# Performance work log

Hardware: AMD Instinct MI355X
Metric: run time of the kernel (lower is better)

Reference implementation:

```python
import jax, jax.numpy as jnp
import numpy as np

B, S, DM, H, HD = 2, 4096, 768, 12, 64
SCALING = HD ** -0.5
LN_EPS = 1e-12
ROPE_BASE = 10000.0


def rotate_half(x):
    x1, x2 = jnp.split(x, 2, axis=-1)
    return jnp.concatenate([-x2, x1], axis=-1)


def setup_inputs() -> dict:
    key = jax.random.key(0)
    ks = jax.random.split(key, 8)
    s = 0.02
    hidden_states = jax.random.normal(ks[0], (B, S, DM), dtype=jnp.float32)
    # true rotary tables: inv_freq over head_dim/2, duplicated (HF convention)
    inv_freq = 1.0 / (ROPE_BASE ** (jnp.arange(0, HD, 2, dtype=jnp.float32) / HD))
    freqs = jnp.arange(S, dtype=jnp.float32)[:, None] * inv_freq[None, :]  # [S, HD/2]
    emb = jnp.concatenate([freqs, freqs], axis=-1)                          # [S, HD]
    cos, sin = jnp.cos(emb), jnp.sin(emb)
    return {
        "hidden_states": hidden_states,
        "cos": cos,
        "sin": sin,
        "Wq": jax.random.normal(ks[1], (DM, DM), dtype=jnp.float32) * s,
        "bq": jnp.zeros((DM,), dtype=jnp.float32),
        "Wk": jax.random.normal(ks[2], (DM, DM), dtype=jnp.float32) * s,
        "bk": jnp.zeros((DM,), dtype=jnp.float32),
        "Wv": jax.random.normal(ks[3], (DM, DM), dtype=jnp.float32) * s,
        "bv": jnp.zeros((DM,), dtype=jnp.float32),
        "Wo": jax.random.normal(ks[4], (DM, DM), dtype=jnp.float32) * s,
        "ln_g": jnp.ones((DM,), dtype=jnp.float32),
        "ln_b": jnp.zeros((DM,), dtype=jnp.float32),
    }


def reference(hidden_states, cos, sin, Wq, bq, Wk, bk, Wv, bv, Wo, ln_g, ln_b):
    # QKV projections -> [B, H, S, HD]
    def proj(W, b):
        return (hidden_states @ W.T + b).reshape(B, S, H, HD).transpose(0, 2, 1, 3)
    q, k, v = proj(Wq, bq), proj(Wk, bk), proj(Wv, bv)

    # RoPE (cos/sin broadcast over batch & heads)
    c = cos[None, None, :, :]
    s_ = sin[None, None, :, :]
    q = q * c + rotate_half(q) * s_
    k = k * c + rotate_half(k) * s_

    # Faithful to source: q pre-scaled, then eager attention scales scores again
    q = q * SCALING
    scores = jnp.einsum("bhsd,bhtd->bhst", q, k) * SCALING  # [B,H,S,S]
    probs = jax.nn.softmax(scores.astype(jnp.float32), axis=-1).astype(v.dtype)
    attn = jnp.einsum("bhst,bhtd->bhsd", probs, v)
    attn = attn.transpose(0, 2, 1, 3).reshape(B, S, DM)

    # output dense (no bias) + residual + LayerNorm
    out = attn @ Wo.T + hidden_states
    mu = jnp.mean(out, axis=-1, keepdims=True)
    var = jnp.var(out, axis=-1, keepdims=True)
    out = (out - mu) * jax.lax.rsqrt(var + LN_EPS) * ln_g + ln_b
    return out
```

## Files before the change

kernel.cpp:

```cpp
#include <hip/hip_runtime.h>
#include <math.h>

#define B_   2
#define S_   4096
#define DM_  768
#define H_   12
#define HD_  64
#define M_   (B_ * S_)
#define ROWELEMS ((size_t)M_ * DM_)
#define WELEMS  ((size_t)DM_ * DM_)

#define QSC (1.4426950408889634f / 64.0f)

typedef unsigned short u16;
typedef unsigned int   u32;
typedef __attribute__((ext_vector_type(8))) short  short8;
typedef __attribute__((ext_vector_type(4))) float  floatx4;
typedef __attribute__((ext_vector_type(4))) u32    uint32x4;

__device__ inline u16 f2bf(float f) {
    u32 u = __builtin_bit_cast(u32, f);
    u += 0x7FFF + ((u >> 16) & 1);
    return (u16)(u >> 16);
}
__device__ inline float bf2f(u16 h) {
    return __builtin_bit_cast(float, (u32)h << 16);
}
__device__ inline u32 pk_trunc(float a, float b) {
    return __builtin_amdgcn_perm(__builtin_bit_cast(u32, b),
                                 __builtin_bit_cast(u32, a), 0x07060302);
}

__device__ inline int sw_off(int r, int cg) {
    return (r << 6) + ((cg ^ (r & 7)) << 3);
}

__device__ __forceinline__ void load_lds16(const u16* g, u16* l) {
    __builtin_amdgcn_global_load_lds(
        (const __attribute__((address_space(1))) u32*)g,
        (__attribute__((address_space(3))) u32*)l, 16, 0, 0);
}

__device__ __forceinline__ void drain_vm() {
    __builtin_amdgcn_s_waitcnt(0x0F70);
}
__device__ __forceinline__ void wait_vm4() {
    __builtin_amdgcn_s_waitcnt(0x0F74);
}

__global__ __launch_bounds__(256) void conv_bf16(
    const float* __restrict__ h,  const float* __restrict__ wq,
    const float* __restrict__ wk, const float* __restrict__ wv,
    const float* __restrict__ wo, u16* __restrict__ hb, u16* __restrict__ wb)
{
    const int y = blockIdx.y;
    const float* src; u16* dst; size_t n4;
    if (y == 0)      { src = h;  dst = hb;              n4 = ROWELEMS / 4; }
    else if (y == 1) { src = wq; dst = wb;              n4 = WELEMS / 4; }
    else if (y == 2) { src = wk; dst = wb + WELEMS;     n4 = WELEMS / 4; }
    else if (y == 3) { src = wv; dst = wb + 2 * WELEMS; n4 = WELEMS / 4; }
    else             { src = wo; dst = wb + 3 * WELEMS; n4 = WELEMS / 4; }
    const size_t stride = (size_t)gridDim.x * 256;
    for (size_t i = blockIdx.x * 256 + threadIdx.x; i < n4; i += stride) {
        float4 v = *(const float4*)&src[i * 4];
        u32 p0 = (u32)f2bf(v.x) | ((u32)f2bf(v.y) << 16);
        u32 p1 = (u32)f2bf(v.z) | ((u32)f2bf(v.w) << 16);
        *(uint2*)&dst[i * 4] = make_uint2(p0, p1);
    }
}

__global__ __launch_bounds__(256, 3) void gemm_qkv(
    const u16* __restrict__ A,
    const u16* __restrict__ W0, const u16* __restrict__ W1, const u16* __restrict__ W2,
    const float* __restrict__ b0, const float* __restrict__ b1, const float* __restrict__ b2,
    const float* __restrict__ cosT, const float* __restrict__ sinT,
    u16* __restrict__ Qh, u16* __restrict__ Kh, u16* __restrict__ Vt)
{
    __shared__ __align__(16) u16 As[128 * 64];
    __shared__ __align__(16) u16 Ws[192 * 64];

    const int tid  = threadIdx.x;
    const int wave = tid >> 6, lane = tid & 63;
    const int n16  = lane & 15, quad = lane >> 4;
    const int m0   = blockIdx.y * 128, n0 = blockIdx.x * 192;
    const int z    = blockIdx.z;

    const u16* Wz = (z == 0) ? W0 : (z == 1) ? W1 : W2;
    const float* bz = (z == 0) ? b0 : (z == 1) ? b1 : b2;

    int gao[4], ldsao[4], gwo[6], ldswo[6];
#pragma unroll
    for (int i = 0; i < 4; i++) {
        int g = wave * 256 + i * 64 + lane;
        int r = g >> 3, cg = (g & 7) ^ (r & 7);
        gao[i]   = r * DM_ + cg * 8;
        ldsao[i] = (wave * 256 + i * 64) * 8;
    }
#pragma unroll
    for (int i = 0; i < 6; i++) {
        int g = wave * 384 + i * 64 + lane;
        int r = g >> 3, cg = (g & 7) ^ (r & 7);
        gwo[i]   = r * DM_ + cg * 8;
        ldswo[i] = (wave * 384 + i * 64) * 8;
    }
    const u16* Ap = A  + (size_t)m0 * DM_;
    const u16* Wp = Wz + (size_t)n0 * DM_;

    floatx4 acc[2][12];
#pragma unroll
    for (int i = 0; i < 2; i++)
#pragma unroll
        for (int j = 0; j < 12; j++) acc[i][j] = (floatx4){0.f, 0.f, 0.f, 0.f};

    for (int k0 = 0; k0 < DM_; k0 += 64) {
        __syncthreads();
#pragma unroll
        for (int i = 0; i < 4; i++)
            load_lds16(Ap + k0 + gao[i], &As[ldsao[i]]);
#pragma unroll
        for (int i = 0; i < 6; i++)
            load_lds16(Wp + k0 + gwo[i], &Ws[ldswo[i]]);
        drain_vm();
        __syncthreads();
#pragma unroll
        for (int ks = 0; ks < 2; ks++) {
            short8 af[2];
#pragma unroll
            for (int t = 0; t < 2; t++)
                af[t] = *(const short8*)&As[sw_off(wave * 32 + t * 16 + n16, ks * 4 + quad)];
#pragma unroll
            for (int jh = 0; jh < 2; jh++) {
                short8 bf[6];
#pragma unroll
                for (int j = 0; j < 6; j++)
                    bf[j] = *(const short8*)&Ws[sw_off((jh * 6 + j) * 16 + n16, ks * 4 + quad)];
#pragma unroll
                for (int i = 0; i < 2; i++)
#pragma unroll
                    for (int j = 0; j < 6; j++)
                        acc[i][jh * 6 + j] = __builtin_amdgcn_mfma_f32_16x16x32_bf16(
                            af[i], bf[j], acc[i][jh * 6 + j], 0, 0, 0);
            }
        }
    }

    if (z == 2) {
#pragma unroll
        for (int i = 0; i < 2; i++)
#pragma unroll
            for (int j = 0; j < 12; j++) {
                const int col = n0 + j * 16 + n16;
                const int h = col >> 6, hd = col & 63;
                const int row0 = m0 + wave * 32 + i * 16 + quad * 4;
                const int b = row0 >> 12, s0 = row0 & 4095;
                const float bias = bz[col];
                float v0 = acc[i][j][0] + bias, v1 = acc[i][j][1] + bias;
                float v2 = acc[i][j][2] + bias, v3 = acc[i][j][3] + bias;
                u32 w0 = (u32)f2bf(v0) | ((u32)f2bf(v1) << 16);
                u32 w1 = (u32)f2bf(v2) | ((u32)f2bf(v3) << 16);
                *(uint2*)&Vt[((size_t)(b * H_ + h) * HD_ + hd) * S_ + s0] = make_uint2(w0, w1);
            }
    } else {
        u32* Out32 = (u32*)((z == 0) ? Qh : Kh);
        const float sc_ = (z == 0) ? QSC : 1.0f;
#pragma unroll
        for (int i = 0; i < 2; i++)
#pragma unroll
            for (int jp = 0; jp < 6; jp++) {
                const int j1 = (jp >> 1) * 4 + (jp & 1);
                const int col1 = n0 + j1 * 16 + n16;
                const int h = col1 >> 6, hd1 = col1 & 63;
                const float bias1 = bz[col1], bias2 = bz[col1 + 32];
#pragma unroll
                for (int r = 0; r < 4; r++) {
                    const int row = m0 + wave * 32 + i * 16 + quad * 4 + r;
                    const int b = row >> 12, s = row & 4095;
                    const float c  = cosT[s * HD_ + hd1];
                    const float sn = sinT[s * HD_ + hd1];
                    const float x1 = acc[i][j1][r] + bias1;
                    const float x2 = acc[i][j1 + 2][r] + bias2;
                    const float y1 = (x1 * c - x2 * sn) * sc_;
                    const float y2 = (x2 * c + x1 * sn) * sc_;
                    Out32[(((size_t)(b * H_ + h) * S_ + s) << 5) + hd1] =
                        (u32)f2bf(y1) | ((u32)f2bf(y2) << 16);
                }
            }
    }
}

__global__ __launch_bounds__(256, 3) void flash_mfma(
    const u16* __restrict__ Qh, const u16* __restrict__ Kh,
    const u16* __restrict__ Vt, u16* __restrict__ O)
{
    __shared__ __align__(16) u16 Ks0[64 * 64];
    __shared__ __align__(16) u16 Vs0[64 * 64];
    __shared__ __align__(16) u16 Ks1[64 * 64];
    __shared__ __align__(16) u16 Vs1[64 * 64];
    __shared__ __align__(16) u16 Ks2[64 * 64];
    __shared__ __align__(16) u16 Vs2[64 * 64];

    const int tid  = threadIdx.x;
    const int wave = tid >> 6, lane = tid & 63;
    const int n16  = lane & 15, quad = lane >> 4;
    const int qt   = blockIdx.x;
    const int bh   = blockIdx.y;
    const size_t qk_base = (size_t)bh * S_ * HD_;
    const size_t vt_base = (size_t)bh * HD_ * S_;
    const int q0   = qt * 128;
    const int wrow = wave * 32;

    short8 qf[2][2];
#pragma unroll
    for (int rt = 0; rt < 2; rt++)
#pragma unroll
        for (int ks = 0; ks < 2; ks++)
            qf[rt][ks] = *(const short8*)&Qh[qk_base +
                (size_t)(q0 + wrow + rt * 16 + n16) * HD_ + ks * 32 + quad * 8];

    short8 ones;
#pragma unroll
    for (int j = 0; j < 8; j++) ones[j] = (short)0x3F80;

    int gk_off[2], gv_off[2], ldso[2];
#pragma unroll
    for (int i = 0; i < 2; i++) {
        int g = wave * 128 + i * 64 + lane;
        int r = g >> 3, cg = (g & 7) ^ (r & 7);
        int rk = (r & 0x23) | ((r & 8) << 1) | ((r & 4) << 1) | ((r & 16) >> 2);
        gk_off[i] = rk * HD_ + cg * 8;
        gv_off[i] = r  * S_  + cg * 8;
        ldso[i]   = (wave * 128 + i * 64) * 8;
    }

    floatx4 o_acc[2][4];
    floatx4 o_l[2];
#pragma unroll
    for (int rt = 0; rt < 2; rt++) {
        o_l[rt] = (floatx4){0.f, 0.f, 0.f, 0.f};
#pragma unroll
        for (int dt = 0; dt < 4; dt++) o_acc[rt][dt] = (floatx4){0.f, 0.f, 0.f, 0.f};
    }

    const u16* Kg = Kh + qk_base;
    const u16* Vg = Vt + vt_base;
#define KT (64 * HD_)

#define STAGE(KSRC, VSRC, KDST, VDST)                                   \
    do {                                                                \
        _Pragma("unroll")                                               \
        for (int i_ = 0; i_ < 2; i_++) {                                \
            load_lds16((KSRC) + gk_off[i_], &(KDST)[ldso[i_]]);         \
            load_lds16((VSRC) + gv_off[i_], &(VDST)[ldso[i_]]);         \
        }                                                               \
    } while (0)

#define COMPUTE_TILE(KSB, VSB)                                          \
    do {                                                                \
        floatx4 sct[4][2];                                              \
        _Pragma("unroll")                                               \
        for (int ct = 0; ct < 4; ct++)                                  \
            _Pragma("unroll")                                           \
            for (int rt = 0; rt < 2; rt++)                              \
                sct[ct][rt] = (floatx4){0.f, 0.f, 0.f, 0.f};            \
        _Pragma("unroll")                                               \
        for (int ks = 0; ks < 2; ks++) {                                \
            short8 kf[4];                                               \
            _Pragma("unroll")                                           \
            for (int ct = 0; ct < 4; ct++)                              \
                kf[ct] = *(const short8*)&(KSB)[sw_off(ct * 16 + n16,   \
                                                       ks * 4 + quad)]; \
            _Pragma("unroll")                                           \
            for (int ct = 0; ct < 4; ct++)                              \
                _Pragma("unroll")                                       \
                for (int rt = 0; rt < 2; rt++)                          \
                    sct[ct][rt] = __builtin_amdgcn_mfma_f32_16x16x32_bf16( \
                        kf[ct], qf[rt][ks], sct[ct][rt], 0, 0, 0);      \
        }                                                               \
        short8 pa[2][2];                                                \
        _Pragma("unroll")                                               \
        for (int rt = 0; rt < 2; rt++)                                  \
            _Pragma("unroll")                                           \
            for (int ks = 0; ks < 2; ks++) {                            \
                const floatx4 lo = sct[2 * ks][rt];                     \
                const floatx4 hi = sct[2 * ks + 1][rt];                 \
                uint32x4 w;                                             \
                w[0] = pk_trunc(__builtin_amdgcn_exp2f(lo[0]),          \
                                __builtin_amdgcn_exp2f(lo[1]));         \
                w[1] = pk_trunc(__builtin_amdgcn_exp2f(lo[2]),          \
                                __builtin_amdgcn_exp2f(lo[3]));         \
                w[2] = pk_trunc(__builtin_amdgcn_exp2f(hi[0]),          \
                                __builtin_amdgcn_exp2f(hi[1]));         \
                w[3] = pk_trunc(__builtin_amdgcn_exp2f(hi[2]),          \
                                __builtin_amdgcn_exp2f(hi[3]));         \
                pa[rt][ks] = __builtin_bit_cast(short8, w);             \
            }                                                           \
        _Pragma("unroll")                                               \
        for (int ks = 0; ks < 2; ks++) {                                \
            short8 vb[4];                                               \
            _Pragma("unroll")                                           \
            for (int dt = 0; dt < 4; dt++)                              \
                vb[dt] = *(const short8*)&(VSB)[sw_off(dt * 16 + n16,   \
                                                       ks * 4 + quad)]; \
            _Pragma("unroll")                                           \
            for (int rt = 0; rt < 2; rt++) {                            \
                _Pragma("unroll")                                       \
                for (int dt = 0; dt < 4; dt++)                          \
                    o_acc[rt][dt] = __builtin_amdgcn_mfma_f32_16x16x32_bf16( \
                        pa[rt][ks], vb[dt], o_acc[rt][dt], 0, 0, 0);    \
                o_l[rt] = __builtin_amdgcn_mfma_f32_16x16x32_bf16(      \
                    pa[rt][ks], ones, o_l[rt], 0, 0, 0);                \
            }                                                           \
        }                                                               \
    } while (0)

    STAGE(Kg,      Vg,      Ks0, Vs0);
    STAGE(Kg + KT, Vg + 64, Ks1, Vs1);

    for (int g = 0; g < 21; ++g) {
        wait_vm4();
        __builtin_amdgcn_s_barrier();
        STAGE(Kg + 2 * KT, Vg + 2 * 64, Ks2, Vs2);
        COMPUTE_TILE(Ks0, Vs0);
        Kg += KT; Vg += 64;

        wait_vm4();
        __builtin_amdgcn_s_barrier();
        STAGE(Kg + 2 * KT, Vg + 2 * 64, Ks0, Vs0);
        COMPUTE_TILE(Ks1, Vs1);
        Kg += KT; Vg += 64;

        wait_vm4();
        __builtin_amdgcn_s_barrier();
        if (g < 20)
            STAGE(Kg + 2 * KT, Vg + 2 * 64, Ks1, Vs1);
        COMPUTE_TILE(Ks2, Vs2);
        Kg += KT; Vg += 64;
    }
    drain_vm();
    __builtin_amdgcn_s_barrier();
    COMPUTE_TILE(Ks0, Vs0);
#undef STAGE
#undef COMPUTE_TILE
#undef KT

    const int b = bh / H_, h = bh % H_;
#pragma unroll
    for (int rt = 0; rt < 2; rt++)
#pragma unroll
        for (int r = 0; r < 4; r++) {
            const float inv = 1.0f / o_l[rt][r];
            const int srow = q0 + wrow + rt * 16 + quad * 4 + r;
            u16* Orow = O + ((size_t)b * S_ + srow) * DM_ + h * HD_;
#pragma unroll
            for (int dt = 0; dt < 4; dt++)
                Orow[dt * 16 + n16] = f2bf(o_acc[rt][dt][r] * inv);
        }
}

__global__ __launch_bounds__(256, 4) void gemm_out(
    const u16* __restrict__ A, const u16* __restrict__ W,
    const float* __restrict__ resid, float* __restrict__ Cf)
{
    __shared__ __align__(16) u16 As[64 * 64];
    __shared__ __align__(16) u16 Ws[128 * 64];

    const int tid  = threadIdx.x;
    const int wave = tid >> 6, lane = tid & 63;
    const int n16  = lane & 15, quad = lane >> 4;
    const int wm   = wave >> 1, wn = wave & 1;
    const int m0   = blockIdx.y * 64, n0 = blockIdx.x * 128;

    int gwo[4], ldswo[4], gao[2], ldsao[2];
#pragma unroll
    for (int i = 0; i < 4; i++) {
        int g = wave * 256 + i * 64 + lane;
        int r = g >> 3, cg = (g & 7) ^ (r & 7);
        gwo[i]   = r * DM_ + cg * 8;
        ldswo[i] = (wave * 256 + i * 64) * 8;
    }
#pragma unroll
    for (int i = 0; i < 2; i++) {
        int g = wave * 128 + i * 64 + lane;
        int r = g >> 3, cg = (g & 7) ^ (r & 7);
        gao[i]   = r * DM_ + cg * 8;
        ldsao[i] = (wave * 128 + i * 64) * 8;
    }
    const u16* Wp = W + (size_t)n0 * DM_;
    const u16* Ap = A + (size_t)m0 * DM_;

    floatx4 acc[2][4];
#pragma unroll
    for (int i = 0; i < 2; i++)
#pragma unroll
        for (int j = 0; j < 4; j++) acc[i][j] = (floatx4){0.f, 0.f, 0.f, 0.f};

    for (int k0 = 0; k0 < DM_; k0 += 64) {
        __syncthreads();
#pragma unroll
        for (int i = 0; i < 4; i++)
            load_lds16(Wp + k0 + gwo[i], &Ws[ldswo[i]]);
#pragma unroll
        for (int i = 0; i < 2; i++)
            load_lds16(Ap + k0 + gao[i], &As[ldsao[i]]);
        drain_vm();
        __syncthreads();

#pragma unroll
        for (int ks = 0; ks < 2; ks++) {
            short8 af[2], bf[4];
#pragma unroll
            for (int rt = 0; rt < 2; rt++)
                af[rt] = *(const short8*)&As[sw_off(wm * 32 + rt * 16 + n16, ks * 4 + quad)];
#pragma unroll
            for (int ct = 0; ct < 4; ct++)
                bf[ct] = *(const short8*)&Ws[sw_off(wn * 64 + ct * 16 + n16, ks * 4 + quad)];
#pragma unroll
            for (int rt = 0; rt < 2; rt++)
#pragma unroll
                for (int ct = 0; ct < 4; ct++)
                    acc[rt][ct] = __builtin_amdgcn_mfma_f32_16x16x32_bf16(
                        af[rt], bf[ct], acc[rt][ct], 0, 0, 0);
        }
    }

#pragma unroll
    for (int rt = 0; rt < 2; rt++)
#pragma unroll
        for (int ct = 0; ct < 4; ct++) {
            const int col = n0 + wn * 64 + ct * 16 + n16;
#pragma unroll
            for (int r = 0; r < 4; r++) {
                const int row = m0 + wm * 32 + rt * 16 + quad * 4 + r;
                Cf[(size_t)row * DM_ + col] = acc[rt][ct][r] + resid[(size_t)row * DM_ + col];
            }
        }
}

__global__ __launch_bounds__(256) void ln_kernel(
    float* __restrict__ io, const float* __restrict__ g, const float* __restrict__ bb)
{
    const int row = blockIdx.x, t = threadIdx.x;
    float* p = io + (size_t)row * DM_;
    float x[3];
    float sum = 0.0f, sq = 0.0f;
#pragma unroll
    for (int i = 0; i < 3; i++) {
        x[i] = p[t + i * 256];
        sum += x[i];
        sq  = fmaf(x[i], x[i], sq);
    }
#pragma unroll
    for (int off = 32; off >= 1; off >>= 1) {
        sum += __shfl_xor(sum, off);
        sq  += __shfl_xor(sq, off);
    }
    __shared__ float s1[4], s2[4];
    if ((t & 63) == 0) { s1[t >> 6] = sum; s2[t >> 6] = sq; }
    __syncthreads();
    sum = s1[0] + s1[1] + s1[2] + s1[3];
    sq  = s2[0] + s2[1] + s2[2] + s2[3];
    const float mu  = sum * (1.0f / 768.0f);
    const float var = sq * (1.0f / 768.0f) - mu * mu;
    const float rs  = rsqrtf(var + 1e-12f);
#pragma unroll
    for (int i = 0; i < 3; i++) {
        const int c = t + i * 256;
        p[c] = (x[i] - mu) * rs * g[c] + bb[c];
    }
}

extern "C" void kernel_launch(void* const* d_in, const int* in_sizes, int n_in,
                              void* d_out, int out_size, void* d_ws, size_t ws_size,
                              hipStream_t stream)
{
    const float* hidden = (const float*)d_in[0];
    const float* cosT   = (const float*)d_in[1];
    const float* sinT   = (const float*)d_in[2];
    const float* Wq     = (const float*)d_in[3];
    const float* bq     = (const float*)d_in[4];
    const float* Wk     = (const float*)d_in[5];
    const float* bk     = (const float*)d_in[6];
    const float* Wv     = (const float*)d_in[7];
    const float* bv     = (const float*)d_in[8];
    const float* Wo     = (const float*)d_in[9];
    const float* ln_g   = (const float*)d_in[10];
    const float* ln_b   = (const float*)d_in[11];
    float* out = (float*)d_out;

    u16* wsb = (u16*)d_ws;
    u16* Hb  = wsb;
    u16* Wb  = wsb + ROWELEMS;
    u16* Qh  = Wb + 4 * WELEMS;
    u16* Kh  = Qh + ROWELEMS;
    u16* Vt  = Kh + ROWELEMS;
    u16* Ob  = Hb;
    u16* Wqb = Wb, *Wkb = Wb + WELEMS, *Wvb = Wb + 2 * WELEMS, *Wob = Wb + 3 * WELEMS;

    conv_bf16<<<dim3(1024, 5), 256, 0, stream>>>(hidden, Wq, Wk, Wv, Wo, Hb, Wb);

    gemm_qkv<<<dim3(DM_ / 192, M_ / 128, 3), 256, 0, stream>>>(
        Hb, Wqb, Wkb, Wvb, bq, bk, bv, cosT, sinT, Qh, Kh, Vt);

    flash_mfma<<<dim3(S_ / 128, B_ * H_), 256, 0, stream>>>(Qh, Kh, Vt, Ob);

    gemm_out<<<dim3(DM_ / 128, M_ / 64), 256, 0, stream>>>(Ob, Wob, hidden, out);

    ln_kernel<<<M_, 256, 0, stream>>>(out, ln_g, ln_b);
}
```

Measured before the change: 265.6 us.

## Double-buffer LDS tiles in QKV and output GEMMs with K=32 stages

Both projection GEMMs move from a single-buffered K=64 loop that fully drains global-to-LDS loads before each compute step to a two-buffer ping-pong with K=32 stages. The next stage's loads are issued before computing on the current buffer, and a partial vmcnt wait replaces the full drain. The LDS layout packs two 32-wide K rows into one 64-element swizzled row to keep reads conflict-free. The aim is to hide global load latency behind MFMA work, at the cost of twice as many barriers per K and smaller per-stage tiles.

```diff
diff --git a/kernel.cpp b/kernel.cpp
--- a/kernel.cpp
+++ b/kernel.cpp
@@ -44,8 +44,14 @@
 __device__ __forceinline__ void drain_vm() {
     __builtin_amdgcn_s_waitcnt(0x0F70);
 }
+__device__ __forceinline__ void wait_vm3() {
+    __builtin_amdgcn_s_waitcnt(0x0F73);
+}
 __device__ __forceinline__ void wait_vm4() {
     __builtin_amdgcn_s_waitcnt(0x0F74);
+}
+__device__ __forceinline__ void wait_vm5() {
+    __builtin_amdgcn_s_waitcnt(0x0F75);
 }
 
 __global__ __launch_bounds__(256) void conv_bf16(
@@ -76,8 +82,10 @@
     const float* __restrict__ cosT, const float* __restrict__ sinT,
     u16* __restrict__ Qh, u16* __restrict__ Kh, u16* __restrict__ Vt)
 {
-    __shared__ __align__(16) u16 As[128 * 64];
-    __shared__ __align__(16) u16 Ws[192 * 64];
+    __shared__ __align__(16) u16 As0[64 * 64];
+    __shared__ __align__(16) u16 As1[64 * 64];
+    __shared__ __align__(16) u16 Ws0[96 * 64];
+    __shared__ __align__(16) u16 Ws1[96 * 64];
 
     const int tid  = threadIdx.x;
     const int wave = tid >> 6, lane = tid & 63;
@@ -88,20 +96,20 @@
     const u16* Wz = (z == 0) ? W0 : (z == 1) ? W1 : W2;
     const float* bz = (z == 0) ? b0 : (z == 1) ? b1 : b2;
 
-    int gao[4], ldsao[4], gwo[6], ldswo[6];
-#pragma unroll
-    for (int i = 0; i < 4; i++) {
-        int g = wave * 256 + i * 64 + lane;
-        int r = g >> 3, cg = (g & 7) ^ (r & 7);
-        gao[i]   = r * DM_ + cg * 8;
-        ldsao[i] = (wave * 256 + i * 64) * 8;
-    }
-#pragma unroll
-    for (int i = 0; i < 6; i++) {
-        int g = wave * 384 + i * 64 + lane;
-        int r = g >> 3, cg = (g & 7) ^ (r & 7);
-        gwo[i]   = r * DM_ + cg * 8;
-        ldswo[i] = (wave * 384 + i * 64) * 8;
+    int gao[2], ldsao[2], gwo[3], ldswo[3];
+#pragma unroll
+    for (int i = 0; i < 2; i++) {
+        int g = wave * 128 + i * 64 + lane;
+        int lr = g >> 3, cg = (g & 7) ^ (lr & 7);
+        gao[i]   = (2 * lr + (cg >> 2)) * DM_ + (cg & 3) * 8;
+        ldsao[i] = g * 8;
+    }
+#pragma unroll
+    for (int i = 0; i < 3; i++) {
+        int g = wave * 192 + i * 64 + lane;
+        int lr = g >> 3, cg = (g & 7) ^ (lr & 7);
+        gwo[i]   = (2 * lr + (cg >> 2)) * DM_ + (cg & 3) * 8;
+        ldswo[i] = g * 8;
     }
     const u16* Ap = A  + (size_t)m0 * DM_;
     const u16* Wp = Wz + (size_t)n0 * DM_;
@@ -112,37 +120,61 @@
 #pragma unroll
         for (int j = 0; j < 12; j++) acc[i][j] = (floatx4){0.f, 0.f, 0.f, 0.f};
 
-    for (int k0 = 0; k0 < DM_; k0 += 64) {
-        __syncthreads();
-#pragma unroll
-        for (int i = 0; i < 4; i++)
-            load_lds16(Ap + k0 + gao[i], &As[ldsao[i]]);
-#pragma unroll
-        for (int i = 0; i < 6; i++)
-            load_lds16(Wp + k0 + gwo[i], &Ws[ldswo[i]]);
-        drain_vm();
-        __syncthreads();
-#pragma unroll
-        for (int ks = 0; ks < 2; ks++) {
-            short8 af[2];
-#pragma unroll
-            for (int t = 0; t < 2; t++)
-                af[t] = *(const short8*)&As[sw_off(wave * 32 + t * 16 + n16, ks * 4 + quad)];
-#pragma unroll
-            for (int jh = 0; jh < 2; jh++) {
-                short8 bf[6];
-#pragma unroll
-                for (int j = 0; j < 6; j++)
-                    bf[j] = *(const short8*)&Ws[sw_off((jh * 6 + j) * 16 + n16, ks * 4 + quad)];
-#pragma unroll
-                for (int i = 0; i < 2; i++)
-#pragma unroll
-                    for (int j = 0; j < 6; j++)
-                        acc[i][jh * 6 + j] = __builtin_amdgcn_mfma_f32_16x16x32_bf16(
-                            af[i], bf[j], acc[i][jh * 6 + j], 0, 0, 0);
-            }
+    const int afr = (n16 >> 1);
+    const int fcg = ((n16 & 1) << 2) | quad;
+
+#define QSTAGE(K0, ADST, WDST)                                          \
+    do {                                                                \
+        _Pragma("unroll")                                               \
+        for (int i_ = 0; i_ < 2; i_++)                                  \
+            load_lds16(Ap + (K0) + gao[i_], &(ADST)[ldsao[i_]]);        \
+        _Pragma("unroll")                                               \
+        for (int i_ = 0; i_ < 3; i_++)                                  \
+            load_lds16(Wp + (K0) + gwo[i_], &(WDST)[ldswo[i_]]);        \
+    } while (0)
+
+#define QCOMPUTE(ASB, WSB)                                              \
+    do {                                                                \
+        short8 af[2];                                                   \
+        _Pragma("unroll")                                               \
+        for (int t_ = 0; t_ < 2; t_++)                                  \
+            af[t_] = *(const short8*)&(ASB)[sw_off(wave * 16 + t_ * 8 + afr, fcg)]; \
+        _Pragma("unroll")                                               \
+        for (int jh = 0; jh < 2; jh++) {                                \
+            short8 bf[6];                                               \
+            _Pragma("unroll")                                           \
+            for (int j_ = 0; j_ < 6; j_++)                              \
+                bf[j_] = *(const short8*)&(WSB)[sw_off((jh * 6 + j_) * 8 + afr, fcg)]; \
+            _Pragma("unroll")                                           \
+            for (int i_ = 0; i_ < 2; i_++)                              \
+                _Pragma("unroll")                                       \
+                for (int j_ = 0; j_ < 6; j_++)                          \
+                    acc[i_][jh * 6 + j_] = __builtin_amdgcn_mfma_f32_16x16x32_bf16( \
+                        af[i_], bf[j_], acc[i_][jh * 6 + j_], 0, 0, 0); \
+        }                                                               \
+    } while (0)
+
+    QSTAGE(0, As0, Ws0);
+
+    for (int t = 0; t < 24; t += 2) {
+        QSTAGE((t + 1) * 32, As1, Ws1);
+        wait_vm5();
+        __syncthreads();
+        QCOMPUTE(As0, Ws0);
+        __syncthreads();
+
+        if (t + 2 < 24) {
+            QSTAGE((t + 2) * 32, As0, Ws0);
+            wait_vm5();
+        } else {
+            drain_vm();
         }
-    }
+        __syncthreads();
+        QCOMPUTE(As1, Ws1);
+        __syncthreads();
+    }
+#undef QSTAGE
+#undef QCOMPUTE
 
     if (z == 2) {
 #pragma unroll
@@ -361,8 +393,10 @@
     const u16* __restrict__ A, const u16* __restrict__ W,
     const float* __restrict__ resid, float* __restrict__ Cf)
 {
-    __shared__ __align__(16) u16 As[64 * 64];
-    __shared__ __align__(16) u16 Ws[128 * 64];
+    __shared__ __align__(16) u16 As0[32 * 64];
+    __shared__ __align__(16) u16 As1[32 * 64];
+    __shared__ __align__(16) u16 Ws0[64 * 64];
+    __shared__ __align__(16) u16 Ws1[64 * 64];
 
     const int tid  = threadIdx.x;
     const int wave = tid >> 6, lane = tid & 63;
@@ -370,20 +404,19 @@
     const int wm   = wave >> 1, wn = wave & 1;
     const int m0   = blockIdx.y * 64, n0 = blockIdx.x * 128;
 
-    int gwo[4], ldswo[4], gao[2], ldsao[2];
-#pragma unroll
-    for (int i = 0; i < 4; i++) {
-        int g = wave * 256 + i * 64 + lane;
-        int r = g >> 3, cg = (g & 7) ^ (r & 7);
-        gwo[i]   = r * DM_ + cg * 8;
-        ldswo[i] = (wave * 256 + i * 64) * 8;
+    int gao, ldsao, gwo[2], ldswo[2];
+    {
+        int g = wave * 64 + lane;
+        int lr = g >> 3, cg = (g & 7) ^ (lr & 7);
+        gao   = (2 * lr + (cg >> 2)) * DM_ + (cg & 3) * 8;
+        ldsao = g * 8;
     }
 #pragma unroll
     for (int i = 0; i < 2; i++) {
         int g = wave * 128 + i * 64 + lane;
-        int r = g >> 3, cg = (g & 7) ^ (r & 7);
-        gao[i]   = r * DM_ + cg * 8;
-        ldsao[i] = (wave * 128 + i * 64) * 8;
+        int lr = g >> 3, cg = (g & 7) ^ (lr & 7);
+        gwo[i]   = (2 * lr + (cg >> 2)) * DM_ + (cg & 3) * 8;
+        ldswo[i] = g * 8;
     }
     const u16* Wp = W + (size_t)n0 * DM_;
     const u16* Ap = A + (size_t)m0 * DM_;
@@ -394,34 +427,55 @@
 #pragma unroll
         for (int j = 0; j < 4; j++) acc[i][j] = (floatx4){0.f, 0.f, 0.f, 0.f};
 
-    for (int k0 = 0; k0 < DM_; k0 += 64) {
-        __syncthreads();
-#pragma unroll
-        for (int i = 0; i < 4; i++)
-            load_lds16(Wp + k0 + gwo[i], &Ws[ldswo[i]]);
-#pragma unroll
-        for (int i = 0; i < 2; i++)
-            load_lds16(Ap + k0 + gao[i], &As[ldsao[i]]);
-        drain_vm();
-        __syncthreads();
-
-#pragma unroll
-        for (int ks = 0; ks < 2; ks++) {
-            short8 af[2], bf[4];
-#pragma unroll
-            for (int rt = 0; rt < 2; rt++)
-                af[rt] = *(const short8*)&As[sw_off(wm * 32 + rt * 16 + n16, ks * 4 + quad)];
-#pragma unroll
-            for (int ct = 0; ct < 4; ct++)
-                bf[ct] = *(const short8*)&Ws[sw_off(wn * 64 + ct * 16 + n16, ks * 4 + quad)];
-#pragma unroll
-            for (int rt = 0; rt < 2; rt++)
-#pragma unroll
-                for (int ct = 0; ct < 4; ct++)
-                    acc[rt][ct] = __builtin_amdgcn_mfma_f32_16x16x32_bf16(
-                        af[rt], bf[ct], acc[rt][ct], 0, 0, 0);
+    const int afr = (n16 >> 1);
+    const int fcg = ((n16 & 1) << 2) | quad;
+
+#define OSTAGE(K0, ADST, WDST)                                          \
+    do {                                                                \
+        load_lds16(Ap + (K0) + gao, &(ADST)[ldsao]);                    \
+        _Pragma("unroll")                                               \
+        for (int i_ = 0; i_ < 2; i_++)                                  \
+            load_lds16(Wp + (K0) + gwo[i_], &(WDST)[ldswo[i_]]);        \
+    } while (0)
+
+#define OCOMPUTE(ASB, WSB)                                              \
+    do {                                                                \
+        short8 af[2], bf[4];                                            \
+        _Pragma("unroll")                                               \
+        for (int rt = 0; rt < 2; rt++)                                  \
+            af[rt] = *(const short8*)&(ASB)[sw_off(wm * 16 + rt * 8 + afr, fcg)]; \
+        _Pragma("unroll")                                               \
+        for (int ct = 0; ct < 4; ct++)                                  \
+            bf[ct] = *(const short8*)&(WSB)[sw_off(wn * 32 + ct * 8 + afr, fcg)]; \
+        _Pragma("unroll")                                               \
+        for (int rt = 0; rt < 2; rt++)                                  \
+            _Pragma("unroll")                                           \
+            for (int ct = 0; ct < 4; ct++)                              \
+                acc[rt][ct] = __builtin_amdgcn_mfma_f32_16x16x32_bf16(  \
+                    af[rt], bf[ct], acc[rt][ct], 0, 0, 0);              \
+    } while (0)
+
+    OSTAGE(0, As0, Ws0);
+
+    for (int t = 0; t < 24; t += 2) {
+        OSTAGE((t + 1) * 32, As1, Ws1);
+        wait_vm3();
+        __syncthreads();
+        OCOMPUTE(As0, Ws0);
+        __syncthreads();
+
+        if (t + 2 < 24) {
+            OSTAGE((t + 2) * 32, As0, Ws0);
+            wait_vm3();
+        } else {
+            drain_vm();
         }
-    }
+        __syncthreads();
+        OCOMPUTE(As1, Ws1);
+        __syncthreads();
+    }
+#undef OSTAGE
+#undef OCOMPUTE
 
 #pragma unroll
     for (int rt = 0; rt < 2; rt++)
```

Result: no change. 266.8 us (+0.5%).
